# Optimization experiments

Measured on AMD Instinct MI355X. Metric: run time of the kernel, lower is better.

## Reference

```python
import jax, jax.numpy as jnp
import numpy as np

C = 64; NET = 32; K = 3; G = 4; GC = C // G; P = K * K
STRIDE = 1; PAD = 1; DIL = 1; OFFSET_SCALE = 1.0
BN_EPS = 1e-5; LN_EPS = 1e-6


def conv2d(x, w, b, groups=1, pad=1):
    # x: (N,C,H,W), w: (O, I//groups, kh, kw)
    y = jax.lax.conv_general_dilated(
        x, w, (1, 1), [(pad, pad), (pad, pad)],
        feature_group_count=groups,
        dimension_numbers=('NCHW', 'OIHW', 'NCHW'))
    return y + b[None, :, None, None]


def dcnv3_core(x, offset, mask):
    """Faithful port of dcnv3_core_pytorch (InternImage).
    x: (N,H,W,C) channels-last; offset: (N,H,W,G*P*2); mask: (N,H,W,G*P) (softmaxed).
    grid_sample(bilinear, zeros padding, align_corners=False) done manually."""
    xp = jnp.pad(x, ((0, 0), (PAD, PAD), (PAD, PAD), (0, 0)))
    N, Hin, Win, _ = xp.shape
    Ho, Wo = offset.shape[1], offset.shape[2]
    # reference points in normalized [0,1] coords (x first, y second)
    start = (DIL * (K - 1)) // 2 + 0.5
    ref_x = (start + jnp.arange(Wo, dtype=jnp.float32) * STRIDE) / Win  # (Wo,)
    ref_y = (start + jnp.arange(Ho, dtype=jnp.float32) * STRIDE) / Hin  # (Ho,)
    ref = jnp.stack(jnp.broadcast_arrays(ref_x[None, :], ref_y[:, None]), axis=-1)  # (Ho,Wo,2)
    # dilation grid (kernel tap offsets, torch meshgrid 'ij' flatten order: w-major)
    kv = (jnp.arange(K, dtype=jnp.float32) * DIL - (DIL * (K - 1)) // 2)
    gx, gy = jnp.meshgrid(kv / Win, kv / Hin, indexing='ij')
    grid = jnp.stack([gx, gy], -1).reshape(P, 2)  # (P,2), same for every group
    # sampling locations, normalized: (N,Ho,Wo,G,P,2)
    off = offset.reshape(N, Ho, Wo, G, P, 2) * (OFFSET_SCALE / jnp.array([Win, Hin], jnp.float32))
    loc = ref[None, :, :, None, None, :] + grid[None, None, None, None, :, :] * OFFSET_SCALE + off
    # grid_sample align_corners=False: pixel = loc*size - 0.5  (since g = 2*loc-1)
    px = loc[..., 0] * Win - 0.5
    py = loc[..., 1] * Hin - 0.5
    x0 = jnp.floor(px); y0 = jnp.floor(py)
    ix0 = x0.astype(jnp.int32); iy0 = y0.astype(jnp.int32)
    wx1 = px - x0; wy1 = py - y0; wx0 = 1.0 - wx1; wy0 = 1.0 - wy1
    xg = xp.reshape(N, Hin, Win, G, GC)
    n_idx = jnp.arange(N)[:, None, None, None, None]
    g_idx = jnp.arange(G)[None, None, None, :, None]

    def sample(ix, iy):
        valid = ((ix >= 0) & (ix < Win) & (iy >= 0) & (iy < Hin)).astype(xg.dtype)
        v = xg[n_idx, jnp.clip(iy, 0, Hin - 1), jnp.clip(ix, 0, Win - 1), g_idx]  # (N,Ho,Wo,G,P,GC)
        return v * valid[..., None]

    val = (sample(ix0, iy0) * (wx0 * wy0)[..., None]
           + sample(ix0 + 1, iy0) * (wx1 * wy0)[..., None]
           + sample(ix0, iy0 + 1) * (wx0 * wy1)[..., None]
           + sample(ix0 + 1, iy0 + 1) * (wx1 * wy1)[..., None])
    out = jnp.einsum('nhwgpc,nhwgp->nhwgc', val, mask.reshape(N, Ho, Wo, G, P))
    return out.reshape(N, Ho, Wo, C)


def setup_inputs() -> dict:
    key = jax.random.key(0)
    ks = jax.random.split(key, 16)
    N, H, W = 4, 128, 128
    f = lambda k, shp, s=1.0: jax.random.normal(k, shp, jnp.float32) * s
    return {
        'input_x': f(ks[0], (N, C, H, W)),
        'input_y': f(ks[1], (N, NET, H, W)),
        'enc_w': f(ks[2], (NET, C), 0.05), 'enc_b': jnp.zeros((NET,), jnp.float32),
        'bn_g': jnp.ones((NET,), jnp.float32), 'bn_b': jnp.zeros((NET,), jnp.float32),
        'bn_m': jnp.zeros((NET,), jnp.float32), 'bn_v': jnp.ones((NET,), jnp.float32),
        'gru_wz': f(ks[3], (NET, 2 * NET, 3, 3), 0.05), 'gru_bz': jnp.zeros((NET,), jnp.float32),
        'gru_wr': f(ks[4], (NET, 2 * NET, 3, 3), 0.05), 'gru_br': jnp.zeros((NET,), jnp.float32),
        'gru_wq': f(ks[5], (NET, 2 * NET, 3, 3), 0.05), 'gru_bq': jnp.zeros((NET,), jnp.float32),
        'dw_w': f(ks[6], (C, 1, 3, 3), 0.1), 'dw_b': jnp.zeros((C,), jnp.float32),
        'ln_g': jnp.ones((C,), jnp.float32), 'ln_b': jnp.zeros((C,), jnp.float32),
        'off_w': f(ks[7], (G * P * 2, C), 0.1), 'off_b': f(ks[8], (G * P * 2,), 0.1),
        'mask_w': f(ks[9], (G * P, C), 0.1), 'mask_b': jnp.zeros((G * P,), jnp.float32),
        'inp_w': f(ks[10], (C, C), 0.1), 'inp_b': jnp.zeros((C,), jnp.float32),
        'out_w': f(ks[11], (C, C), 0.1), 'out_b': jnp.zeros((C,), jnp.float32),
    }


def reference(input_x, input_y, enc_w, enc_b, bn_g, bn_b, bn_m, bn_v,
              gru_wz, gru_bz, gru_wr, gru_br, gru_wq, gru_bq,
              dw_w, dw_b, ln_g, ln_b, off_w, off_b, mask_w, mask_b,
              inp_w, inp_b, out_w, out_b):
    N, _, H, W = input_x.shape
    # encoder: 1x1 Conv + BN(eval) + SiLU
    e = jnp.einsum('nchw,oc->nohw', input_x, enc_w) + enc_b[None, :, None, None]
    e = (e - bn_m[None, :, None, None]) * jax.lax.rsqrt(bn_v + BN_EPS)[None, :, None, None]
    e = e * bn_g[None, :, None, None] + bn_b[None, :, None, None]
    x_en = jax.nn.silu(e)
    # ConvGRU: h' = (1-z)*h + z*q
    hx = jnp.concatenate([input_y, x_en], axis=1)
    z = jax.nn.sigmoid(conv2d(hx, gru_wz, gru_bz))
    r = jax.nn.sigmoid(conv2d(hx, gru_wr, gru_br))
    q = jnp.tanh(conv2d(jnp.concatenate([r * input_y, x_en], axis=1), gru_wq, gru_bq))
    h = (1.0 - z) * input_y + z * q  # (N,NET,H,W)
    # channels-last main path
    inp = input_x.transpose(0, 2, 3, 1)  # (N,H,W,C)
    x = inp @ inp_w.T + inp_b
    # depthwise conv on gru state -> LN (channels_last) -> GELU
    y = conv2d(h, dw_w, dw_b, groups=NET).transpose(0, 2, 3, 1)  # (N,H,W,C)
    mu = y.mean(-1, keepdims=True)
    var = ((y - mu) ** 2).mean(-1, keepdims=True)
    y = (y - mu) * jax.lax.rsqrt(var + LN_EPS) * ln_g + ln_b
    y = jax.nn.gelu(y, approximate=False)
    offset = y @ off_w.T + off_b  # (N,H,W,G*P*2)
    m = y @ mask_w.T + mask_b
    m = jax.nn.softmax(m.reshape(N, H, W, G, P), axis=-1).reshape(N, H, W, G * P)
    x = dcnv3_core(x, offset, m)
    x = x @ out_w.T + out_b
    return jax.nn.silu(x.transpose(0, 3, 1, 2)), h
```

## Files before the change

### kernel.cpp

```cpp
#include <hip/hip_runtime.h>
#include <hip/hip_bf16.h>

typedef __hip_bfloat16 bf16;
typedef short short8v __attribute__((ext_vector_type(8)));
typedef short short4v __attribute__((ext_vector_type(4)));
typedef float float4v __attribute__((ext_vector_type(4)));

static __device__ __forceinline__ float b2f(bf16 v){ return __bfloat162float(v); }
static __device__ __forceinline__ bf16 f2b(float v){ return __float2bfloat16(v); }
static __device__ __forceinline__ float bu2f(unsigned short u){ return __uint_as_float(((unsigned)u) << 16); }
static __device__ __forceinline__ short f2bs(float v){ bf16 t = __float2bfloat16(v); return *(short*)&t; }

#define WT 128
#define HWT 16384

#define OFF_BZ    20544
#define OFF_BR    39008
#define OFF_BQ    57472
#define OFF_DWP   57504
#define OFF_DWB   58080
#define OFF_LNG   58144
#define OFF_LNB   58208
#define OFF_OMB   65184
#define OFF_WINP  65296
#define OFF_BINP  69392
#define OFF_BOUT  73552
#define NW_TOTAL  73616
#define NBF_ZR    36864
#define NBF_Q     18432
#define NBF_OM    7168
#define NBF_OUT   4096
#define NPREP     (NW_TOTAL + NBF_ZR + NBF_Q + NBF_OM + NBF_OUT)
#define NHALO     2064
#define NTOT      (NPREP + NHALO)
#define NB_PREPB  556

#define B_WZRB  294912
#define B_WQB   368640
#define B_WOMB  405504
#define B_WOUTB 419840
#define B_HXP   428544
#define B_QINP  9081344
#define B_ZBUF  17734144
#define B_XL    428544

__global__ void __launch_bounds__(256) k_stage1(
    const float* __restrict__ enc_w, const float* __restrict__ enc_b,
    const float* __restrict__ bn_g, const float* __restrict__ bn_b,
    const float* __restrict__ bn_m, const float* __restrict__ bn_v,
    const float* __restrict__ gwz, const float* __restrict__ gbz,
    const float* __restrict__ gwr, const float* __restrict__ gbr,
    const float* __restrict__ gwq, const float* __restrict__ gbq,
    const float* __restrict__ dww, const float* __restrict__ dwb,
    const float* __restrict__ lng, const float* __restrict__ lnb,
    const float* __restrict__ offw, const float* __restrict__ offb,
    const float* __restrict__ maskw, const float* __restrict__ maskb,
    const float* __restrict__ inpw, const float* __restrict__ inpb,
    const float* __restrict__ outw, const float* __restrict__ outb,
    float* __restrict__ Wp, bf16* __restrict__ wzrb, bf16* __restrict__ wqb,
    bf16* __restrict__ womb, bf16* __restrict__ woutb,
    bf16* __restrict__ hxp, bf16* __restrict__ qinp,
    const float* __restrict__ X, const float* __restrict__ Y) {
  __shared__ float xls[4096];
  __shared__ float ewls[2048];
  __shared__ float escl[64];
  int tid = threadIdx.x;
  int b = blockIdx.x;

  if (b < NB_PREPB) {
    int i = b * 256 + tid;
    if (i >= NTOT) return;
    if (i >= NPREP) {
      int t = i - NPREP;
      int img = t / 516, r = t % 516;
      int ph, pw;
      if (r < 130) { ph = 0; pw = r; }
      else if (r < 260) { ph = 129; pw = r - 130; }
      else if (r < 388) { ph = r - 260 + 1; pw = 0; }
      else { ph = r - 388 + 1; pw = 129; }
      size_t pb = (((size_t)img * 130 + ph) * 130 + pw) * 64;
      uint4 zz = make_uint4(0, 0, 0, 0);
      #pragma unroll
      for (int k = 0; k < 8; ++k) {
        ((uint4*)(hxp + pb))[k] = zz;
        ((uint4*)(qinp + pb))[k] = zz;
      }
      return;
    }
    if (i >= NW_TOTAL) {
      int d = i - NW_TOTAL;
      if (d < NBF_ZR) {
        int t = d / 9216, rem = d % 9216;
        int kc = rem / 512, rem2 = rem % 512;
        int ln = rem2 >> 3, j = rem2 & 7;
        int n = t * 16 + (ln & 15);
        int cin = (kc & 1) * 32 + ((ln >> 4) << 3) + j;
        int tap = kc >> 1;
        float v = (n < 32) ? gwz[(n*64 + cin)*9 + tap] : gwr[((n-32)*64 + cin)*9 + tap];
        wzrb[d] = f2b(v);
      } else if (d < NBF_ZR + NBF_Q) {
        int d2 = d - NBF_ZR;
        int t = d2 / 9216, rem = d2 % 9216;
        int kc = rem / 512, rem2 = rem % 512;
        int ln = rem2 >> 3, j = rem2 & 7;
        int n = t * 16 + (ln & 15);
        int cin = (kc & 1) * 32 + ((ln >> 4) << 3) + j;
        int tap = kc >> 1;
        wqb[d2] = f2b(gwq[(n*64 + cin)*9 + tap]);
      } else if (d < NBF_ZR + NBF_Q + NBF_OM) {
        int d3 = d - NBF_ZR - NBF_Q;
        int wv = d3 / 1024, rem = d3 % 1024;
        int kc = rem / 512, rem2 = rem % 512;
        int ln = rem2 >> 3, j = rem2 & 7;
        int jcol = wv * 16 + (ln & 15);
        int c = kc * 32 + ((ln >> 4) << 3) + j;
        float v = (jcol < 72) ? offw[jcol*64 + c] : ((jcol < 108) ? maskw[(jcol-72)*64 + c] : 0.f);
        womb[d3] = f2b(v);
      } else {
        int d4 = d - NBF_ZR - NBF_Q - NBF_OM;
        int nt = d4 / 1024, rem = d4 % 1024;
        int kc = rem / 512, rem2 = rem % 512;
        int ln = rem2 >> 3, j = rem2 & 7;
        int o = nt * 16 + (ln & 15);
        int c = kc * 32 + ((ln >> 4) << 3) + j;
        woutb[d4] = f2b(outw[o*64 + c]);
      }
      return;
    }
    float v;
    if (i < 20544) { v = 0.f; }
    else if (i < 20576) { v = gbz[i - OFF_BZ]; }
    else if (i < 39008) { v = 0.f; }
    else if (i < 39040) { v = gbr[i - OFF_BR]; }
    else if (i < 57472) { v = 0.f; }
    else if (i < 57504) { v = gbq[i - OFF_BQ]; }
    else if (i < 58080) { int d = i - OFF_DWP; int tap = d >> 6, o = d & 63; v = dww[o*9 + tap]; }
    else if (i < 58144) { v = dwb[i - OFF_DWB]; }
    else if (i < 58208) { v = lng[i - OFF_LNG]; }
    else if (i < 58272) { v = lnb[i - OFF_LNB]; }
    else if (i < 65184) { v = 0.f; }
    else if (i < 65292) { int j = i - OFF_OMB; v = (j < 72) ? offb[j] : maskb[j-72]; }
    else if (i < 65296) { v = 0.f; }
    else if (i < 69392) { int d = i - OFF_WINP; int c = d >> 6, o = d & 63; v = inpw[o*64 + c]; }
    else if (i < 69456) { v = inpb[i - OFF_BINP]; }
    else if (i < 73552) { v = 0.f; }
    else { v = outb[i - OFF_BOUT]; }
    Wp[i] = v;
    return;
  }

  int pb2 = b - NB_PREPB;
  int img = pb2 >> 8, h = (pb2 >> 1) & 127, w0 = (pb2 & 1) * 64;
  int px = tid & 63, sect = tid >> 6;
  #pragma unroll
  for (int k = 0; k < 8; ++k) {
    int i2 = k * 256 + tid;
    int c = i2 >> 5, o = i2 & 31;
    ewls[i2] = enc_w[o*64 + c];
  }
  if (tid < 32) {
    float sc = bn_g[tid] * rsqrtf(bn_v[tid] + 1e-5f);
    escl[tid] = sc;
    escl[32 + tid] = (enc_b[tid] - bn_m[tid]) * sc + bn_b[tid];
  }
  int hw = h * WT + w0 + px;
  const float* xp = X + (size_t)img * (64 * HWT) + hw;
  #pragma unroll
  for (int i2 = 0; i2 < 16; ++i2) {
    int c = sect * 16 + i2;
    xls[c * 64 + px] = xp[c * HWT];
  }
  const float* yp = Y + (size_t)img * (32 * HWT) + hw;
  bf16 yv[8];
  #pragma unroll
  for (int i2 = 0; i2 < 8; ++i2) yv[i2] = f2b(yp[(sect * 8 + i2) * HWT]);
  size_t pbb = (((size_t)img * 130 + h + 1) * 130 + (w0 + px + 1)) * 64;
  *(uint4*)(hxp + pbb + sect * 8) = *(const uint4*)yv;
  __syncthreads();
  float aen[8];
  #pragma unroll
  for (int o = 0; o < 8; ++o) aen[o] = 0.f;
  for (int k = 0; k < 64; ++k) {
    float a = xls[k * 64 + px];
    const float* we = ewls + k * 32 + sect * 8;
    #pragma unroll
    for (int o = 0; o < 8; ++o) aen[o] += a * we[o];
  }
  bf16 xe[8];
  #pragma unroll
  for (int o = 0; o < 8; ++o) {
    int oo = sect * 8 + o;
    float e = aen[o] * escl[oo] + escl[32 + oo];
    xe[o] = f2b(e / (1.f + __expf(-e)));
  }
  *(uint4*)(hxp + pbb + 32 + sect * 8) = *(const uint4*)xe;
  *(uint4*)(qinp + pbb + 32 + sect * 8) = *(const uint4*)xe;
}

__global__ void __launch_bounds__(256) k_zr(
    const float* __restrict__ Wp,
    const bf16* __restrict__ hxp, const bf16* __restrict__ wzrb,
    bf16* __restrict__ qinp, bf16* __restrict__ zbuf) {
  __shared__ short zt[32 * 132];
  __shared__ short ryt[128 * 40];
  int tid = threadIdx.x;
  int wv = tid >> 6, ln = tid & 63;
  int quad = ln >> 4, lm = ln & 15;
  int img = blockIdx.z, h = blockIdx.y;
  int p0 = wv * 32;
  const short* hs = (const short*)hxp;
  const short* ws = (const short*)wzrb;
  size_t rowb = ((size_t)img * 130 + h + 1) * 130;
  const short* ab0 = hs + (rowb + p0 + lm + 1) * 64 + quad * 8;
  const short* ab1 = ab0 + 16 * 64;
  short8v a0[18], a1[18];
  #pragma unroll
  for (int kc = 0; kc < 18; ++kc) {
    const int tap = kc >> 1, cin0 = (kc & 1) * 32;
    const int dd = (tap / 3 - 1) * 130 + (tap % 3 - 1);
    a0[kc] = *(const short8v*)(ab0 + dd * 64 + cin0);
    a1[kc] = *(const short8v*)(ab1 + dd * 64 + cin0);
  }
  float4v acc[8];
  #pragma unroll
  for (int t = 0; t < 8; ++t) acc[t] = (float4v){0.f, 0.f, 0.f, 0.f};
  #pragma unroll
  for (int kc = 0; kc < 18; ++kc) {
    #pragma unroll
    for (int t = 0; t < 4; ++t) {
      short8v b = *(const short8v*)(ws + ((t * 18 + kc) * 64 + ln) * 8);
      acc[t*2]   = __builtin_amdgcn_mfma_f32_16x16x32_bf16(a0[kc], b, acc[t*2], 0, 0, 0);
      acc[t*2+1] = __builtin_amdgcn_mfma_f32_16x16x32_bf16(a1[kc], b, acc[t*2+1], 0, 0, 0);
    }
  }
  #pragma unroll
  for (int mt = 0; mt < 2; ++mt) {
    #pragma unroll
    for (int t = 0; t < 2; ++t) {
      int n = t * 16 + lm;
      float bz = Wp[OFF_BZ + n];
      short zp[4];
      #pragma unroll
      for (int ri = 0; ri < 4; ++ri)
        zp[ri] = f2bs(1.f / (1.f + __expf(-(acc[t*2+mt][ri] + bz))));
      *(short4v*)(zt + n * 132 + p0 + mt * 16 + quad * 4) = *(const short4v*)zp;
    }
  }
  #pragma unroll
  for (int mt = 0; mt < 2; ++mt) {
    #pragma unroll
    for (int t = 2; t < 4; ++t) {
      int c = (t - 2) * 16 + lm;
      float br = Wp[OFF_BR + c];
      #pragma unroll
      for (int ri = 0; ri < 4; ++ri) {
        int px = p0 + mt * 16 + quad * 4 + ri;
        float rv = 1.f / (1.f + __expf(-(acc[t*2+mt][ri] + br)));
        float yy = b2f(hxp[(rowb + px + 1) * 64 + c]);
        ryt[px * 40 + c] = f2bs(rv * yy);
      }
    }
  }
  __syncthreads();
  {
    int n2 = tid >> 3, pq = tid & 7;
    short8v z0 = *(const short8v*)(zt + n2 * 132 + pq * 16);
    short8v z1 = *(const short8v*)(zt + n2 * 132 + pq * 16 + 8);
    short* zo = (short*)zbuf + (((size_t)img * 128 + h) * 32 + n2) * 128 + pq * 16;
    *(short8v*)zo = z0;
    *(short8v*)(zo + 8) = z1;
  }
  {
    int px = tid >> 1, chalf = tid & 1;
    short8v r0 = *(const short8v*)(ryt + px * 40 + chalf * 16);
    short8v r1 = *(const short8v*)(ryt + px * 40 + chalf * 16 + 8);
    short* qo = (short*)qinp + (rowb + px + 1) * 64 + chalf * 16;
    *(short8v*)qo = r0;
    *(short8v*)(qo + 8) = r1;
  }
}

__global__ void __launch_bounds__(256) k_stageB(
    const float* __restrict__ Y, const float* __restrict__ Wp,
    const bf16* __restrict__ qinp, const bf16* __restrict__ wqb,
    const bf16* __restrict__ zbuf, float* __restrict__ outh,
    const float* __restrict__ X, bf16* __restrict__ xl) {
  __shared__ char sm[16896];
  int tid = threadIdx.x;
  int b = blockIdx.x;

  if (b < 512) {
    float* hout = (float*)sm;
    int wv = tid >> 6, ln = tid & 63;
    int quad = ln >> 4, lm = ln & 15;
    int img = b >> 7, h = b & 127;
    int p0 = wv * 32;
    const short* qs = (const short*)qinp;
    const short* ws = (const short*)wqb;
    size_t rowb = ((size_t)img * 130 + h + 1) * 130;
    const short* ab0 = qs + (rowb + p0 + lm + 1) * 64 + quad * 8;
    const short* ab1 = ab0 + 16 * 64;
    float4v acc[4];
    #pragma unroll
    for (int t = 0; t < 4; ++t) acc[t] = (float4v){0.f, 0.f, 0.f, 0.f};
    #pragma unroll
    for (int kc = 0; kc < 18; ++kc) {
      const int tap = kc >> 1, cin0 = (kc & 1) * 32;
      const int dd = (tap / 3 - 1) * 130 + (tap % 3 - 1);
      short8v a0 = *(const short8v*)(ab0 + dd * 64 + cin0);
      short8v a1 = *(const short8v*)(ab1 + dd * 64 + cin0);
      #pragma unroll
      for (int t = 0; t < 2; ++t) {
        short8v bb = *(const short8v*)(ws + ((t * 18 + kc) * 64 + ln) * 8);
        acc[t*2]   = __builtin_amdgcn_mfma_f32_16x16x32_bf16(a0, bb, acc[t*2], 0, 0, 0);
        acc[t*2+1] = __builtin_amdgcn_mfma_f32_16x16x32_bf16(a1, bb, acc[t*2+1], 0, 0, 0);
      }
    }
    #pragma unroll
    for (int mt = 0; mt < 2; ++mt) {
      #pragma unroll
      for (int t = 0; t < 2; ++t) {
        int n = t * 16 + lm;
        float bq = Wp[OFF_BQ + n];
        float4 hv;
        hv.x = acc[t*2+mt][0] + bq; hv.y = acc[t*2+mt][1] + bq;
        hv.z = acc[t*2+mt][2] + bq; hv.w = acc[t*2+mt][3] + bq;
        *(float4*)(hout + n * 132 + p0 + mt * 16 + quad * 4) = hv;
      }
    }
    __syncthreads();
    const short* zbb = (const short*)zbuf + ((size_t)img * 128 + h) * 32 * 128;
    #pragma unroll
    for (int r = 0; r < 4; ++r) {
      int n = (tid >> 5) + r * 8;
      int px4 = (tid & 31) * 4;
      float4 hv = *(const float4*)(hout + n * 132 + px4);
      uint2 zz = *(const uint2*)(zbb + n * 128 + px4);
      size_t gb = ((size_t)img * 32 + n) * HWT + h * 128 + px4;
      float4 yv = *(const float4*)(Y + gb);
      float z0 = bu2f((unsigned short)(zz.x & 0xFFFFu)), z1 = bu2f((unsigned short)(zz.x >> 16));
      float z2 = bu2f((unsigned short)(zz.y & 0xFFFFu)), z3 = bu2f((unsigned short)(zz.y >> 16));
      float4 o;
      o.x = (1.f - z0) * yv.x + z0 * tanhf(hv.x);
      o.y = (1.f - z1) * yv.y + z1 * tanhf(hv.y);
      o.z = (1.f - z2) * yv.z + z2 * tanhf(hv.z);
      o.w = (1.f - z3) * yv.w + z3 * tanhf(hv.w);
      *(float4*)(outh + gb) = o;
    }
    return;
  }

  {
    float* xls = (float*)sm;
    int b2 = b - 512;
    int px = tid & 63, sect = tid >> 6;
    int img = b2 >> 8, h = (b2 >> 1) & 127, w0 = (b2 & 1) * 64;
    int hw = h * WT + w0 + px;
    const float* xp = X + (size_t)img * (64 * HWT) + hw;
    #pragma unroll
    for (int i = 0; i < 16; ++i) {
      int c = sect * 16 + i;
      xls[c * 64 + px] = xp[c * HWT];
    }
    __syncthreads();
    float acc[16];
    #pragma unroll
    for (int o = 0; o < 16; ++o) acc[o] = Wp[OFF_BINP + sect * 16 + o];
    for (int k = 0; k < 64; ++k) {
      float a = xls[k * 64 + px];
      const float* wr = Wp + OFF_WINP + k * 64 + sect * 16;
      #pragma unroll
      for (int o = 0; o < 16; ++o) acc[o] += a * wr[o];
    }
    bf16 ov[16];
    #pragma unroll
    for (int o = 0; o < 16; ++o) ov[o] = f2b(acc[o]);
    bf16* op = xl + ((size_t)img * HWT + hw) * 64 + sect * 16;
    ((uint4*)op)[0] = ((const uint4*)ov)[0];
    ((uint4*)op)[1] = ((const uint4*)ov)[1];
  }
}

#define LDS_PSA  0
#define LDS_PSB  2048
#define LDS_STAT 4096
#define LDS_Y    4608
#define LDS_OM   13824
#define LDS_TOT  28416

__global__ void __launch_bounds__(512) k_mega(
    const float* __restrict__ Wp, const float* __restrict__ hb,
    const bf16* __restrict__ xl, const bf16* __restrict__ womb,
    const bf16* __restrict__ woutb, float* __restrict__ out0) {
  __shared__ char smem[LDS_TOT];
  float* psa  = (float*)(smem + LDS_PSA);
  float* psb  = (float*)(smem + LDS_PSB);
  float* stat = (float*)(smem + LDS_STAT);
  short* yls  = (short*)(smem + LDS_Y);
  short* omls = (short*)(smem + LDS_OM);
  short* vls  = (short*)(smem + LDS_Y);

  int tid = threadIdx.x;
  int bid = blockIdx.x;
  int xcd = bid & 7, slot = bid >> 3;
  int img = slot >> 5;
  int rem = slot & 31;
  int h = xcd * 16 + (rem & 15);
  int w0 = (rem >> 4) * 64;

  int wloc = tid & 63, part = tid >> 6;
  int w = w0 + wloc;
  float yv[8];
  {
    const float* hn = hb + (size_t)img * (32 * HWT);
    #pragma unroll
    for (int i = 0; i < 8; ++i) yv[i] = Wp[OFF_DWB + part*8 + i];
    #pragma unroll
    for (int tap = 0; tap < 9; ++tap) {
      int dy = tap / 3 - 1, dx = tap % 3 - 1;
      int hh = h + dy, ww = w + dx;
      bool ok = ((unsigned)hh < 128u) && ((unsigned)ww < 128u);
      int off = hh * WT + ww;
      #pragma unroll
      for (int j = 0; j < 4; ++j) {
        int cin = part * 4 + j;
        float a = ok ? hn[cin * HWT + off] : 0.f;
        yv[2*j]   += a * Wp[OFF_DWP + tap*64 + part*8 + 2*j];
        yv[2*j+1] += a * Wp[OFF_DWP + tap*64 + part*8 + 2*j+1];
      }
    }
  }
  float lsum = 0.f, lsq = 0.f;
  #pragma unroll
  for (int i = 0; i < 8; ++i) { lsum += yv[i]; lsq += yv[i]*yv[i]; }
  psa[part * 64 + wloc] = lsum;
  psb[part * 64 + wloc] = lsq;
  __syncthreads();
  if (tid < 64) {
    float s = 0.f, q = 0.f;
    #pragma unroll
    for (int p = 0; p < 8; ++p) { s += psa[p*64 + tid]; q += psb[p*64 + tid]; }
    float mu = s * (1.f/64.f);
    float var = q * (1.f/64.f) - mu * mu;
    stat[tid*2] = mu;
    stat[tid*2+1] = rsqrtf(var + 1e-6f);
  }
  __syncthreads();
  {
    float mu = stat[wloc*2], inv = stat[wloc*2+1];
    bf16 tmp[8];
    #pragma unroll
    for (int i = 0; i < 8; ++i) {
      int c = part*8 + i;
      float v = (yv[i] - mu) * inv * Wp[OFF_LNG + c] + Wp[OFF_LNB + c];
      tmp[i] = f2b(0.5f * v * (1.f + erff(v * 0.70710678118654752f)));
    }
    *(short8v*)(yls + wloc*72 + part*8) = *(const short8v*)tmp;
  }
  __syncthreads();

  int wv = tid >> 6, ln = tid & 63, quad = ln >> 4, lm = ln & 15;
  if (wv < 7) {
    const short* wb = (const short*)womb;
    float4v acc[4];
    #pragma unroll
    for (int mt = 0; mt < 4; ++mt) acc[mt] = (float4v){0.f,0.f,0.f,0.f};
    #pragma unroll
    for (int kc = 0; kc < 2; ++kc) {
      short8v b = *(const short8v*)(wb + ((wv * 2 + kc) * 64 + ln) * 8);
      #pragma unroll
      for (int mt = 0; mt < 4; ++mt) {
        short8v a = *(const short8v*)(yls + (mt*16 + lm)*72 + kc*32 + quad*8);
        acc[mt] = __builtin_amdgcn_mfma_f32_16x16x32_bf16(a, b, acc[mt], 0, 0, 0);
      }
    }
    float bias = Wp[OFF_OMB + wv*16 + lm];
    #pragma unroll
    for (int mt = 0; mt < 4; ++mt) {
      #pragma unroll
      for (int ri = 0; ri < 4; ++ri)
        omls[(mt*16 + quad*4 + ri)*114 + wv*16 + lm] = f2bs(acc[mt][ri] + bias);
    }
  }
  __syncthreads();

  {
    int px = tid >> 3, g = (tid >> 1) & 3, half = tid & 1;
    const short* oml = omls + px*114;
    float m[9];
    #pragma unroll
    for (int p = 0; p < 9; ++p) m[p] = bu2f((unsigned short)oml[72 + g*9 + p]);
    float mx = m[0];
    #pragma unroll
    for (int p = 1; p < 9; ++p) mx = fmaxf(mx, m[p]);
    float sum = 0.f;
    #pragma unroll
    for (int p = 0; p < 9; ++p) { m[p] = __expf(m[p] - mx); sum += m[p]; }
    float rs = 1.f / sum;
    int wg = w0 + px;
    const bf16* xn = xl + (size_t)img * (HWT * 64);
    float acc[8];
    #pragma unroll
    for (int i = 0; i < 8; ++i) acc[i] = 0.f;
    for (int p = 0; p < 9; ++p) {
      float bx = (float)(wg + p / 3 - 1);
      float by = (float)(h + p % 3 - 1);
      float ox = bu2f((unsigned short)oml[g*18 + p*2]);
      float oy = bu2f((unsigned short)oml[g*18 + p*2 + 1]);
      float mk = m[p] * rs;
      float pxx = bx + ox, pyy = by + oy;
      float fx = floorf(pxx), fy = floorf(pyy);
      int jx0 = (int)fx, jy0 = (int)fy;
      float wx1 = pxx - fx, wy1 = pyy - fy;
      float wx0 = 1.f - wx1, wy0 = 1.f - wy1;
      int cjx[4] = { jx0, jx0 + 1, jx0, jx0 + 1 };
      int cjy[4] = { jy0, jy0, jy0 + 1, jy0 + 1 };
      float cw[4] = { wx0*wy0, wx1*wy0, wx0*wy1, wx1*wy1 };
      #pragma unroll
      for (int k = 0; k < 4; ++k) {
        if ((unsigned)cjx[k] < 128u && (unsigned)cjy[k] < 128u) {
          float cf = mk * cw[k];
          const bf16* s = xn + (size_t)(cjy[k] * WT + cjx[k]) * 64 + g * 16 + half * 8;
          uint4 u0 = *(const uint4*)(s);
          const unsigned uu[4] = {u0.x,u0.y,u0.z,u0.w};
          #pragma unroll
          for (int q = 0; q < 4; ++q) {
            acc[2*q]     += cf * bu2f((unsigned short)(uu[q] & 0xFFFFu));
            acc[2*q + 1] += cf * bu2f((unsigned short)(uu[q] >> 16));
          }
        }
      }
    }
    bf16 tmp[8];
    #pragma unroll
    for (int i = 0; i < 8; ++i) tmp[i] = f2b(acc[i]);
    *(short8v*)(vls + px*72 + g*16 + half*8) = *(const short8v*)tmp;
  }
  __syncthreads();

  {
    const short* wb = (const short*)woutb;
    #pragma unroll
    for (int s = 0; s < 2; ++s) {
      int tile = wv * 2 + s;
      int nt = tile >> 2, mt = tile & 3;
      float4v acc = (float4v){0.f,0.f,0.f,0.f};
      #pragma unroll
      for (int kc = 0; kc < 2; ++kc) {
        short8v b = *(const short8v*)(wb + ((nt * 2 + kc) * 64 + ln) * 8);
        short8v a = *(const short8v*)(vls + (mt*16 + lm)*72 + kc*32 + quad*8);
        acc = __builtin_amdgcn_mfma_f32_16x16x32_bf16(a, b, acc, 0, 0, 0);
      }
      int ch = nt*16 + lm;
      float bias = Wp[OFF_BOUT + ch];
      float4 v;
      float s0 = acc[0] + bias; v.x = s0 / (1.f + __expf(-s0));
      float s1 = acc[1] + bias; v.y = s1 / (1.f + __expf(-s1));
      float s2 = acc[2] + bias; v.z = s2 / (1.f + __expf(-s2));
      float s3 = acc[3] + bias; v.w = s3 / (1.f + __expf(-s3));
      *(float4*)(out0 + ((size_t)img*64 + ch)*HWT + h*128 + w0 + mt*16 + quad*4) = v;
    }
  }
}

extern "C" void kernel_launch(void* const* d_in, const int* in_sizes, int n_in,
                              void* d_out, int out_size, void* d_ws, size_t ws_size,
                              hipStream_t stream) {
  const float* input_x = (const float*)d_in[0];
  const float* input_y = (const float*)d_in[1];

  float* Wp = (float*)d_ws;
  bf16* WZRB  = (bf16*)((char*)d_ws + B_WZRB);
  bf16* WQB   = (bf16*)((char*)d_ws + B_WQB);
  bf16* WOMB  = (bf16*)((char*)d_ws + B_WOMB);
  bf16* WOUTB = (bf16*)((char*)d_ws + B_WOUTB);
  bf16* HXP   = (bf16*)((char*)d_ws + B_HXP);
  bf16* QINP  = (bf16*)((char*)d_ws + B_QINP);
  bf16* ZBUF  = (bf16*)((char*)d_ws + B_ZBUF);
  bf16* XL    = (bf16*)((char*)d_ws + B_XL);
  float* out0 = (float*)d_out;
  float* outh = (float*)d_out + 4194304;

  k_stage1<<<dim3(NB_PREPB + 1024), dim3(256), 0, stream>>>(
      (const float*)d_in[2], (const float*)d_in[3], (const float*)d_in[4], (const float*)d_in[5],
      (const float*)d_in[6], (const float*)d_in[7], (const float*)d_in[8], (const float*)d_in[9],
      (const float*)d_in[10], (const float*)d_in[11], (const float*)d_in[12], (const float*)d_in[13],
      (const float*)d_in[14], (const float*)d_in[15], (const float*)d_in[16], (const float*)d_in[17],
      (const float*)d_in[18], (const float*)d_in[19], (const float*)d_in[20], (const float*)d_in[21],
      (const float*)d_in[22], (const float*)d_in[23], (const float*)d_in[24], (const float*)d_in[25],
      Wp, WZRB, WQB, WOMB, WOUTB, HXP, QINP, input_x, input_y);
  k_zr<<<dim3(1, 128, 4), dim3(256), 0, stream>>>(Wp, HXP, WZRB, QINP, ZBUF);
  k_stageB<<<dim3(1536), dim3(256), 0, stream>>>(input_y, Wp, QINP, WQB, ZBUF, outh, input_x, XL);
  k_mega<<<dim3(1024), dim3(512), 0, stream>>>(Wp, outh, XL, WOMB, WOUTB, out0);
}
```

Before: 245.1 us.

## Move input projection to MFMA, rebalance stageB blocks with XCD-aware mapping

```diff
diff --git a/kernel.cpp b/kernel.cpp
--- a/kernel.cpp
+++ b/kernel.cpp
@@ -10,10 +10,12 @@
 static __device__ __forceinline__ bf16 f2b(float v){ return __float2bfloat16(v); }
 static __device__ __forceinline__ float bu2f(unsigned short u){ return __uint_as_float(((unsigned)u) << 16); }
 static __device__ __forceinline__ short f2bs(float v){ bf16 t = __float2bfloat16(v); return *(short*)&t; }
+static __device__ __forceinline__ float ftanh(float x){ return 1.f - 2.f / (1.f + __expf(2.f * x)); }
 
 #define WT 128
 #define HWT 16384
 
+#define OFF_WINPB 1024
 #define OFF_BZ    20544
 #define OFF_BR    39008
 #define OFF_BQ    57472
@@ -128,7 +130,17 @@
       return;
     }
     float v;
-    if (i < 20544) { v = 0.f; }
+    if (i < 20544) {
+      if (i >= OFF_WINPB && i < OFF_WINPB + 2048) {
+        int d0 = (i - OFF_WINPB) * 2;
+        int nt = d0 >> 10, kc = (d0 >> 9) & 1, lnn = (d0 >> 3) & 63, j0 = d0 & 7;
+        int o = nt * 16 + (lnn & 15);
+        int c = kc * 32 + ((lnn >> 4) << 3) + j0;
+        unsigned lo = (unsigned)(unsigned short)f2bs(inpw[o * 64 + c]);
+        unsigned hi = (unsigned)(unsigned short)f2bs(inpw[o * 64 + c + 1]);
+        v = __uint_as_float(lo | (hi << 16));
+      } else v = 0.f;
+    }
     else if (i < 20576) { v = gbz[i - OFF_BZ]; }
     else if (i < 39008) { v = 0.f; }
     else if (i < 39040) { v = gbr[i - OFF_BR]; }
@@ -285,99 +297,93 @@
     const bf16* __restrict__ qinp, const bf16* __restrict__ wqb,
     const bf16* __restrict__ zbuf, float* __restrict__ outh,
     const float* __restrict__ X, bf16* __restrict__ xl) {
-  __shared__ char sm[16896];
+  __shared__ short xs[64 * 72];
   int tid = threadIdx.x;
-  int b = blockIdx.x;
-
-  if (b < 512) {
-    float* hout = (float*)sm;
-    int wv = tid >> 6, ln = tid & 63;
-    int quad = ln >> 4, lm = ln & 15;
-    int img = b >> 7, h = b & 127;
-    int p0 = wv * 32;
+  int bid = blockIdx.x;
+  int xcd = bid & 7, u = bid >> 3;
+  int part = u & 1, slot = u >> 1;
+  int img = slot >> 5, rem = slot & 31;
+  int hh = xcd * 16 + (rem & 15);
+  int w0 = (rem >> 4) * 64;
+  int wv = tid >> 6, ln = tid & 63, quad = ln >> 4, lm = ln & 15;
+
+  if (part == 0) {
+    int p0 = w0 + wv * 16;
     const short* qs = (const short*)qinp;
     const short* ws = (const short*)wqb;
-    size_t rowb = ((size_t)img * 130 + h + 1) * 130;
-    const short* ab0 = qs + (rowb + p0 + lm + 1) * 64 + quad * 8;
-    const short* ab1 = ab0 + 16 * 64;
-    float4v acc[4];
-    #pragma unroll
-    for (int t = 0; t < 4; ++t) acc[t] = (float4v){0.f, 0.f, 0.f, 0.f};
+    size_t rowb = ((size_t)img * 130 + hh + 1) * 130;
+    const short* ab = qs + (rowb + p0 + lm + 1) * 64 + quad * 8;
+    float4v acc0 = (float4v){0.f,0.f,0.f,0.f};
+    float4v acc1 = (float4v){0.f,0.f,0.f,0.f};
     #pragma unroll
     for (int kc = 0; kc < 18; ++kc) {
       const int tap = kc >> 1, cin0 = (kc & 1) * 32;
       const int dd = (tap / 3 - 1) * 130 + (tap % 3 - 1);
-      short8v a0 = *(const short8v*)(ab0 + dd * 64 + cin0);
-      short8v a1 = *(const short8v*)(ab1 + dd * 64 + cin0);
-      #pragma unroll
-      for (int t = 0; t < 2; ++t) {
-        short8v bb = *(const short8v*)(ws + ((t * 18 + kc) * 64 + ln) * 8);
-        acc[t*2]   = __builtin_amdgcn_mfma_f32_16x16x32_bf16(a0, bb, acc[t*2], 0, 0, 0);
-        acc[t*2+1] = __builtin_amdgcn_mfma_f32_16x16x32_bf16(a1, bb, acc[t*2+1], 0, 0, 0);
-      }
-    }
-    #pragma unroll
-    for (int mt = 0; mt < 2; ++mt) {
-      #pragma unroll
-      for (int t = 0; t < 2; ++t) {
-        int n = t * 16 + lm;
-        float bq = Wp[OFF_BQ + n];
-        float4 hv;
-        hv.x = acc[t*2+mt][0] + bq; hv.y = acc[t*2+mt][1] + bq;
-        hv.z = acc[t*2+mt][2] + bq; hv.w = acc[t*2+mt][3] + bq;
-        *(float4*)(hout + n * 132 + p0 + mt * 16 + quad * 4) = hv;
-      }
-    }
-    __syncthreads();
-    const short* zbb = (const short*)zbuf + ((size_t)img * 128 + h) * 32 * 128;
-    #pragma unroll
-    for (int r = 0; r < 4; ++r) {
-      int n = (tid >> 5) + r * 8;
-      int px4 = (tid & 31) * 4;
-      float4 hv = *(const float4*)(hout + n * 132 + px4);
-      uint2 zz = *(const uint2*)(zbb + n * 128 + px4);
-      size_t gb = ((size_t)img * 32 + n) * HWT + h * 128 + px4;
+      short8v a  = *(const short8v*)(ab + dd * 64 + cin0);
+      short8v b0 = *(const short8v*)(ws + ((0 * 18 + kc) * 64 + ln) * 8);
+      short8v b1 = *(const short8v*)(ws + ((1 * 18 + kc) * 64 + ln) * 8);
+      acc0 = __builtin_amdgcn_mfma_f32_16x16x32_bf16(a, b0, acc0, 0, 0, 0);
+      acc1 = __builtin_amdgcn_mfma_f32_16x16x32_bf16(a, b1, acc1, 0, 0, 0);
+    }
+    int px4 = p0 + quad * 4;
+    #pragma unroll
+    for (int t = 0; t < 2; ++t) {
+      float4v acc = t ? acc1 : acc0;
+      int n = t * 16 + lm;
+      float bq = Wp[OFF_BQ + n];
+      size_t gb = ((size_t)img * 32 + n) * HWT + hh * 128 + px4;
+      uint2 zz = *(const uint2*)((const short*)zbuf + (((size_t)img * 128 + hh) * 32 + n) * 128 + px4);
       float4 yv = *(const float4*)(Y + gb);
       float z0 = bu2f((unsigned short)(zz.x & 0xFFFFu)), z1 = bu2f((unsigned short)(zz.x >> 16));
       float z2 = bu2f((unsigned short)(zz.y & 0xFFFFu)), z3 = bu2f((unsigned short)(zz.y >> 16));
       float4 o;
-      o.x = (1.f - z0) * yv.x + z0 * tanhf(hv.x);
-      o.y = (1.f - z1) * yv.y + z1 * tanhf(hv.y);
-      o.z = (1.f - z2) * yv.z + z2 * tanhf(hv.z);
-      o.w = (1.f - z3) * yv.w + z3 * tanhf(hv.w);
+      o.x = (1.f - z0) * yv.x + z0 * ftanh(acc[0] + bq);
+      o.y = (1.f - z1) * yv.y + z1 * ftanh(acc[1] + bq);
+      o.z = (1.f - z2) * yv.z + z2 * ftanh(acc[2] + bq);
+      o.w = (1.f - z3) * yv.w + z3 * ftanh(acc[3] + bq);
       *(float4*)(outh + gb) = o;
     }
     return;
   }
 
   {
-    float* xls = (float*)sm;
-    int b2 = b - 512;
-    int px = tid & 63, sect = tid >> 6;
-    int img = b2 >> 8, h = (b2 >> 1) & 127, w0 = (b2 & 1) * 64;
-    int hw = h * WT + w0 + px;
-    const float* xp = X + (size_t)img * (64 * HWT) + hw;
-    #pragma unroll
-    for (int i = 0; i < 16; ++i) {
-      int c = sect * 16 + i;
-      xls[c * 64 + px] = xp[c * HWT];
+    const float* xb = X + (size_t)img * (64 * HWT) + hh * 128 + w0 + wv * 16 + lm;
+    short8v a[2];
+    #pragma unroll
+    for (int kc = 0; kc < 2; ++kc) {
+      short tmp[8];
+      #pragma unroll
+      for (int j = 0; j < 8; ++j)
+        tmp[j] = f2bs(xb[(size_t)(kc * 32 + quad * 8 + j) * HWT]);
+      a[kc] = *(const short8v*)tmp;
+    }
+    const short* wib = (const short*)Wp + 2 * OFF_WINPB;
+    float4v acc[4];
+    #pragma unroll
+    for (int nt = 0; nt < 4; ++nt) acc[nt] = (float4v){0.f,0.f,0.f,0.f};
+    #pragma unroll
+    for (int kc = 0; kc < 2; ++kc) {
+      #pragma unroll
+      for (int nt = 0; nt < 4; ++nt) {
+        short8v b = *(const short8v*)(wib + ((nt * 2 + kc) * 64 + ln) * 8);
+        acc[nt] = __builtin_amdgcn_mfma_f32_16x16x32_bf16(a[kc], b, acc[nt], 0, 0, 0);
+      }
+    }
+    #pragma unroll
+    for (int nt = 0; nt < 4; ++nt) {
+      int o = nt * 16 + lm;
+      float bias = Wp[OFF_BINP + o];
+      #pragma unroll
+      for (int ri = 0; ri < 4; ++ri)
+        xs[(wv * 16 + quad * 4 + ri) * 72 + o] = f2bs(acc[nt][ri] + bias);
     }
     __syncthreads();
-    float acc[16];
-    #pragma unroll
-    for (int o = 0; o < 16; ++o) acc[o] = Wp[OFF_BINP + sect * 16 + o];
-    for (int k = 0; k < 64; ++k) {
-      float a = xls[k * 64 + px];
-      const float* wr = Wp + OFF_WINP + k * 64 + sect * 16;
-      #pragma unroll
-      for (int o = 0; o < 16; ++o) acc[o] += a * wr[o];
-    }
-    bf16 ov[16];
-    #pragma unroll
-    for (int o = 0; o < 16; ++o) ov[o] = f2b(acc[o]);
-    bf16* op = xl + ((size_t)img * HWT + hw) * 64 + sect * 16;
-    ((uint4*)op)[0] = ((const uint4*)ov)[0];
-    ((uint4*)op)[1] = ((const uint4*)ov)[1];
+    int row = tid >> 2, c0 = (tid & 3) * 16;
+    short8v v0 = *(const short8v*)(xs + row * 72 + c0);
+    short8v v1 = *(const short8v*)(xs + row * 72 + c0 + 8);
+    short* op = (short*)xl + ((size_t)img * HWT + hh * 128 + w0 + row) * 64 + c0;
+    *(short8v*)op = v0;
+    *(short8v*)(op + 8) = v1;
   }
 }
 
@@ -590,6 +596,6 @@
       (const float*)d_in[22], (const float*)d_in[23], (const float*)d_in[24], (const float*)d_in[25],
       Wp, WZRB, WQB, WOMB, WOUTB, HXP, QINP, input_x, input_y);
   k_zr<<<dim3(1, 128, 4), dim3(256), 0, stream>>>(Wp, HXP, WZRB, QINP, ZBUF);
-  k_stageB<<<dim3(1536), dim3(256), 0, stream>>>(input_y, Wp, QINP, WQB, ZBUF, outh, input_x, XL);
+  k_stageB<<<dim3(2048), dim3(256), 0, stream>>>(input_y, Wp, QINP, WQB, ZBUF, outh, input_x, XL);
   k_mega<<<dim3(1024), dim3(512), 0, stream>>>(Wp, outh, XL, WOMB, WOUTB, out0);
 }
```

Result: faster. 225.5 us (-8.0%).
